# Performance work log

Hardware: AMD Instinct MI355X
Metric: run time of the kernel (lower is better)

## Reference

```python
import jax, jax.numpy as jnp
import numpy as np

N = 8192          # num nodes
F_IN = 512        # num_features
H = 256           # hidden_dim
D = 64            # embedding_dim
E = 262144        # num edges (avg degree 32)


def setup_inputs() -> dict:
    key = jax.random.key(0)
    ks = jax.random.split(key, 6)
    x = jax.random.normal(ks[0], (N, F_IN), dtype=jnp.float32)
    adj_rows = jax.random.randint(ks[1], (E,), 0, N)
    adj_cols = jax.random.randint(ks[2], (E,), 0, N)
    adj_vals = jax.random.uniform(ks[3], (E,), dtype=jnp.float32)
    W1 = jax.random.normal(ks[4], (F_IN, H), dtype=jnp.float32) / np.sqrt(F_IN)
    b1 = jnp.zeros((H,), dtype=jnp.float32)
    W2 = jax.random.normal(ks[5], (H, D), dtype=jnp.float32) / np.sqrt(H)
    b2 = jnp.zeros((D,), dtype=jnp.float32)
    return {"x": x, "adj_rows": adj_rows, "adj_cols": adj_cols,
            "adj_vals": adj_vals, "W1": W1, "b1": b1, "W2": W2, "b2": b2}


def _spmm(rows, cols, vals, dense):
    # sparse [N,N] @ dense [N,F] via gather + segment-sum (COO spmm)
    gathered = vals[:, None] * dense[cols]           # [E, F]
    return jax.ops.segment_sum(gathered, rows, num_segments=N)


def reference(x, adj_rows, adj_cols, adj_vals, W1, b1, W2, b2):
    # GCN layer 1: linear -> spmm -> relu (dropout is identity in eval mode)
    h = _spmm(adj_rows, adj_cols, adj_vals, x @ W1 + b1)   # [N, H]
    h = jax.nn.relu(h)
    # GCN layer 2: linear -> spmm
    z = _spmm(adj_rows, adj_cols, adj_vals, h @ W2 + b2)   # [N, D]
    # decode: sigmoid(z z^T)
    adj_rec = jax.nn.sigmoid(z @ z.T)                       # [N, N]
    return (z, adj_rec)
```

## Files before the change

kernel.cpp:

```cpp
#include <hip/hip_runtime.h>
#include <hip/hip_bf16.h>

#define NN 8192
#define FIN 512
#define HD 256
#define DD 64
#define NE 262144
#define BCAP 128

typedef __bf16 bf16_t;
typedef __bf16 bf16x8 __attribute__((ext_vector_type(8)));
typedef __bf16 bf16x4 __attribute__((ext_vector_type(4)));
typedef float f32x4 __attribute__((ext_vector_type(4)));

__global__ __launch_bounds__(256) void prep_kernel(const float* __restrict__ x, bf16_t* __restrict__ x_b,
                                                   const float* __restrict__ W1, bf16_t* __restrict__ w1t,
                                                   const float* __restrict__ W2, bf16_t* __restrict__ w2t,
                                                   int* __restrict__ deg) {
    int b = blockIdx.x;
    if (b < 4096) {
        int i = (b * 256 + threadIdx.x) * 4;
        float4 v = *reinterpret_cast<const float4*>(x + i);
        x_b[i + 0] = (bf16_t)v.x;
        x_b[i + 1] = (bf16_t)v.y;
        x_b[i + 2] = (bf16_t)v.z;
        x_b[i + 3] = (bf16_t)v.w;
    } else if (b < 4096 + 512) {
        int o = (b - 4096) * 256 + threadIdx.x;
        int r = o & 511;
        int c = o >> 9;
        w1t[o] = (bf16_t)W1[r * HD + c];
    } else if (b < 4096 + 512 + 64) {
        int o = (b - 4096 - 512) * 256 + threadIdx.x;
        int r = o & 255;
        int c = o >> 8;
        w2t[o] = (bf16_t)W2[r * DD + c];
    } else {
        int o = (b - 4096 - 512 - 64) * 256 + threadIdx.x;
        deg[o] = 0;
    }
}


__global__ void scatter_edges(const int* __restrict__ rows, const int* __restrict__ cols,
                              const float* __restrict__ vals,
                              int* __restrict__ deg, int2* __restrict__ sedge) {
    int e = blockIdx.x * blockDim.x + threadIdx.x;
    if (e < NE) {
        int r = rows[e];
        int p = atomicAdd(&deg[r], 1);
        int2 pk;
        pk.x = cols[e];
        pk.y = __float_as_int(vals[e]);
        sedge[r * BCAP + p] = pk;
    }
}


__global__ __launch_bounds__(256) void spmm_h_kernel(const int* __restrict__ deg,
                                                     const int2* __restrict__ sedge,
                                                     const bf16_t* __restrict__ h0,
                                                     bf16_t* __restrict__ h) {
    int wv = threadIdx.x >> 6;
    int lane = threadIdx.x & 63;
    int r = blockIdx.x * 4 + wv;
    int nd = deg[r];
    int base = r * BCAP;
    __shared__ int2 ecS[4][64];
    float a0 = 0.f, a1 = 0.f, a2 = 0.f, a3 = 0.f;
    for (int e0 = 0; e0 < nd; e0 += 64) {
        int rem = nd - e0;
        if (rem > 64) rem = 64;
        if (lane < rem) ecS[wv][lane] = sedge[base + e0 + lane];
#pragma unroll 4
        for (int e = 0; e < rem; e++) {
            int c = ecS[wv][e].x;
            float v = __int_as_float(ecS[wv][e].y);
            bf16x4 hv = *reinterpret_cast<const bf16x4*>(h0 + (size_t)c * HD + lane * 4);
            a0 += v * (float)hv[0];
            a1 += v * (float)hv[1];
            a2 += v * (float)hv[2];
            a3 += v * (float)hv[3];
        }
    }
    bf16x4 o;
    o[0] = (bf16_t)fmaxf(a0, 0.f);
    o[1] = (bf16_t)fmaxf(a1, 0.f);
    o[2] = (bf16_t)fmaxf(a2, 0.f);
    o[3] = (bf16_t)fmaxf(a3, 0.f);
    *reinterpret_cast<bf16x4*>(h + (size_t)r * HD + lane * 4) = o;
}

__global__ __launch_bounds__(256) void spmm_z_kernel(const int* __restrict__ deg,
                                                     const int2* __restrict__ sedge,
                                                     const bf16_t* __restrict__ z0,
                                                     float* __restrict__ z_out,
                                                     bf16_t* __restrict__ z_b) {
    int wv = threadIdx.x >> 6;
    int lane = threadIdx.x & 63;
    int r = blockIdx.x * 4 + wv;
    int sub = lane >> 4;
    int fl = lane & 15;
    int nd = deg[r];
    int base = r * BCAP;
    __shared__ int2 ecS[4][64];
    float a0 = 0.f, a1 = 0.f, a2 = 0.f, a3 = 0.f;
    for (int e0 = 0; e0 < nd; e0 += 64) {
        int rem = nd - e0;
        if (rem > 64) rem = 64;
        if (lane < rem) ecS[wv][lane] = sedge[base + e0 + lane];
#pragma unroll 4
        for (int e = sub; e < rem; e += 4) {
            int c = ecS[wv][e].x;
            float v = __int_as_float(ecS[wv][e].y);
            bf16x4 zv = *reinterpret_cast<const bf16x4*>(z0 + (size_t)c * DD + fl * 4);
            a0 += v * (float)zv[0];
            a1 += v * (float)zv[1];
            a2 += v * (float)zv[2];
            a3 += v * (float)zv[3];
        }
    }
    a0 += __shfl_xor(a0, 16); a0 += __shfl_xor(a0, 32);
    a1 += __shfl_xor(a1, 16); a1 += __shfl_xor(a1, 32);
    a2 += __shfl_xor(a2, 16); a2 += __shfl_xor(a2, 32);
    a3 += __shfl_xor(a3, 16); a3 += __shfl_xor(a3, 32);
    if (sub == 0) {
        f32x4 o = {a0, a1, a2, a3};
        *reinterpret_cast<f32x4*>(z_out + (size_t)r * DD + fl * 4) = o;
        bf16x4 ob;
        ob[0] = (bf16_t)a0; ob[1] = (bf16_t)a1; ob[2] = (bf16_t)a2; ob[3] = (bf16_t)a3;
        *reinterpret_cast<bf16x4*>(z_b + (size_t)r * DD + fl * 4) = ob;
    }
}

template <int ACT, typename OutT, int MW, int NT>
__global__ __launch_bounds__(256) void gemm_bt(const bf16_t* __restrict__ A,
                                               const bf16_t* __restrict__ Bt,
                                               const float* __restrict__ bias,
                                               OutT* __restrict__ C,
                                               int M, int N, int K) {
    int wave = threadIdx.x >> 6;
    int lane = threadIdx.x & 63;
    int lr = lane & 15;
    int lq = lane >> 4;
    int bm = (ACT == 2) ? blockIdx.y : blockIdx.x;
    int bn = (ACT == 2) ? blockIdx.x : blockIdx.y;
    int mblk = bm * (64 * MW);
    int m0 = mblk + wave * (16 * MW);
    int n0 = bn * (16 * NT);

    f32x4 acc[MW][NT];
#pragma unroll
    for (int i = 0; i < MW; i++)
#pragma unroll
        for (int t = 0; t < NT; t++) acc[i][t] = {0.f, 0.f, 0.f, 0.f};

    const bf16_t* Abase = A + (size_t)(m0 + lr) * K + lq * 8;
    const bf16_t* Bbase = Bt + (size_t)(n0 + lr) * K + lq * 8;

    for (int k0 = 0; k0 < K; k0 += 32) {
        bf16x8 a[MW];
#pragma unroll
        for (int i = 0; i < MW; i++)
            a[i] = *reinterpret_cast<const bf16x8*>(Abase + (size_t)i * 16 * K + k0);
#pragma unroll
        for (int t = 0; t < NT; t++) {
            bf16x8 b = *reinterpret_cast<const bf16x8*>(Bbase + (size_t)t * 16 * K + k0);
#pragma unroll
            for (int i = 0; i < MW; i++)
                acc[i][t] = __builtin_amdgcn_mfma_f32_16x16x32_bf16(a[i], b, acc[i][t], 0, 0, 0);
        }
    }

    if (ACT == 2) {
        __shared__ float ldsT[4][16][65];
        int c4 = (lane & 15) * 4;
        int rr = lane >> 4;
#pragma unroll
        for (int i = 0; i < MW; i++) {
#pragma unroll
            for (int t = 0; t < 4; t++)
#pragma unroll
                for (int r = 0; r < 4; r++) {
                    float v = acc[i][t][r];
                    v = 1.f / (1.f + __expf(-v));
                    ldsT[wave][lq * 4 + r][t * 16 + lr] = v;
                }
#pragma unroll
            for (int j = 0; j < 4; j++) {
                int row_l = j * 4 + rr;
                f32x4 v = *reinterpret_cast<const f32x4*>(&ldsT[wave][row_l][c4]);
                size_t grow = (size_t)(m0 + i * 16 + row_l);
                *reinterpret_cast<f32x4*>(&C[grow * N + n0 + c4]) = v;
            }
        }
    } else {
#pragma unroll
        for (int i = 0; i < MW; i++) {
#pragma unroll
            for (int t = 0; t < NT; t++) {
                int col = n0 + t * 16 + lr;
                float bv = bias ? bias[col] : 0.f;
#pragma unroll
                for (int r = 0; r < 4; r++) {
                    int row = m0 + i * 16 + lq * 4 + r;
                    C[(size_t)row * N + col] = (OutT)(acc[i][t][r] + bv);
                }
            }
        }
    }
}


extern "C" void kernel_launch(void* const* d_in, const int* in_sizes, int n_in,
                              void* d_out, int out_size, void* d_ws, size_t ws_size,
                              hipStream_t stream) {
    const float* x   = (const float*)d_in[0];
    const int* rows  = (const int*)d_in[1];
    const int* cols  = (const int*)d_in[2];
    const float* vals = (const float*)d_in[3];
    const float* W1  = (const float*)d_in[4];
    const float* b1  = (const float*)d_in[5];
    const float* W2  = (const float*)d_in[6];
    const float* b2  = (const float*)d_in[7];

    float* out_z   = (float*)d_out;
    float* out_adj = out_z + (size_t)NN * DD;

    char* ws = (char*)d_ws;
    size_t off = 0;
    auto alloc = [&](size_t bytes) { void* p = ws + off; off += (bytes + 255) & ~(size_t)255; return p; };
    bf16_t* x_b   = (bf16_t*)alloc((size_t)NN * FIN * 2);
    bf16_t* w1t   = (bf16_t*)alloc((size_t)HD * FIN * 2);
    bf16_t* w2t   = (bf16_t*)alloc((size_t)DD * HD * 2);
    bf16_t* h0    = (bf16_t*)alloc((size_t)NN * HD * 2);
    bf16_t* h_b   = (bf16_t*)alloc((size_t)NN * HD * 2);
    bf16_t* z0    = (bf16_t*)alloc((size_t)NN * DD * 2);
    bf16_t* z_b   = (bf16_t*)alloc((size_t)NN * DD * 2);
    int* deg      = (int*)alloc((size_t)NN * 4);
    int2* sedge   = (int2*)alloc((size_t)NN * BCAP * 8);

    prep_kernel<<<4096 + 512 + 64 + 32, 256, 0, stream>>>(x, x_b, W1, w1t, W2, w2t, deg);

    scatter_edges<<<NE / 256, 256, 0, stream>>>(rows, cols, vals, deg, sedge);

    gemm_bt<0, bf16_t, 1, 4><<<dim3(NN / 64, HD / 64), 256, 0, stream>>>(x_b, w1t, b1, h0, NN, HD, FIN);

    spmm_h_kernel<<<NN / 4, 256, 0, stream>>>(deg, sedge, h0, h_b);

    gemm_bt<0, bf16_t, 1, 4><<<dim3(NN / 64, DD / 64), 256, 0, stream>>>(h_b, w2t, b2, z0, NN, DD, HD);

    spmm_z_kernel<<<NN / 4, 256, 0, stream>>>(deg, sedge, z0, out_z, z_b);

    gemm_bt<2, float, 2, 4><<<dim3(NN / 64, NN / 128), 256, 0, stream>>>(z_b, z_b, nullptr, out_adj, NN, NN, DD);
}
```

Baseline: 368.3 us.

## Fuse first-layer SpMM with second-layer GEMM via shared-memory tile and MFMA

Merges the layer-1 SpMM+ReLU kernel with the h@W2+b2 GEMM. Each block now aggregates 16 rows into shared memory and multiplies them by W2 with bf16 MFMA instructions. This removes the h intermediate's write and read through global memory and one kernel launch. In exchange there are 4x fewer blocks, each wave processes 4 rows serially, and a block barrier sits before the GEMM, which could reduce latency hiding in the gather.

Result: no change. 369.8 us (+0.4%).

```diff
diff --git a/kernel.cpp b/kernel.cpp
--- a/kernel.cpp
+++ b/kernel.cpp
@@ -56,39 +56,65 @@
     }
 }
 
-
-__global__ __launch_bounds__(256) void spmm_h_kernel(const int* __restrict__ deg,
-                                                     const int2* __restrict__ sedge,
-                                                     const bf16_t* __restrict__ h0,
-                                                     bf16_t* __restrict__ h) {
+__global__ __launch_bounds__(256) void spmm_h_gemm2_kernel(const int* __restrict__ deg,
+                                                           const int2* __restrict__ sedge,
+                                                           const bf16_t* __restrict__ h0,
+                                                           const bf16_t* __restrict__ w2t,
+                                                           const float* __restrict__ b2,
+                                                           bf16_t* __restrict__ z0) {
     int wv = threadIdx.x >> 6;
     int lane = threadIdx.x & 63;
-    int r = blockIdx.x * 4 + wv;
-    int nd = deg[r];
-    int base = r * BCAP;
+    int r0 = blockIdx.x * 16;
     __shared__ int2 ecS[4][64];
-    float a0 = 0.f, a1 = 0.f, a2 = 0.f, a3 = 0.f;
-    for (int e0 = 0; e0 < nd; e0 += 64) {
-        int rem = nd - e0;
-        if (rem > 64) rem = 64;
-        if (lane < rem) ecS[wv][lane] = sedge[base + e0 + lane];
+    __shared__ bf16_t hS[16][264];
+
+#pragma unroll
+    for (int i = 0; i < 4; i++) {
+        int r = r0 + wv * 4 + i;
+        int nd = deg[r];
+        int base = r * BCAP;
+        float a0 = 0.f, a1 = 0.f, a2 = 0.f, a3 = 0.f;
+        for (int e0 = 0; e0 < nd; e0 += 64) {
+            int rem = nd - e0;
+            if (rem > 64) rem = 64;
+            if (lane < rem) ecS[wv][lane] = sedge[base + e0 + lane];
 #pragma unroll 4
-        for (int e = 0; e < rem; e++) {
-            int c = ecS[wv][e].x;
-            float v = __int_as_float(ecS[wv][e].y);
-            bf16x4 hv = *reinterpret_cast<const bf16x4*>(h0 + (size_t)c * HD + lane * 4);
-            a0 += v * (float)hv[0];
-            a1 += v * (float)hv[1];
-            a2 += v * (float)hv[2];
-            a3 += v * (float)hv[3];
-        }
-    }
-    bf16x4 o;
-    o[0] = (bf16_t)fmaxf(a0, 0.f);
-    o[1] = (bf16_t)fmaxf(a1, 0.f);
-    o[2] = (bf16_t)fmaxf(a2, 0.f);
-    o[3] = (bf16_t)fmaxf(a3, 0.f);
-    *reinterpret_cast<bf16x4*>(h + (size_t)r * HD + lane * 4) = o;
+            for (int e = 0; e < rem; e++) {
+                int c = ecS[wv][e].x;
+                float v = __int_as_float(ecS[wv][e].y);
+                bf16x4 hv = *reinterpret_cast<const bf16x4*>(h0 + (size_t)c * HD + lane * 4);
+                a0 += v * (float)hv[0];
+                a1 += v * (float)hv[1];
+                a2 += v * (float)hv[2];
+                a3 += v * (float)hv[3];
+            }
+        }
+        bf16x4 o;
+        o[0] = (bf16_t)fmaxf(a0, 0.f);
+        o[1] = (bf16_t)fmaxf(a1, 0.f);
+        o[2] = (bf16_t)fmaxf(a2, 0.f);
+        o[3] = (bf16_t)fmaxf(a3, 0.f);
+        *reinterpret_cast<bf16x4*>(&hS[wv * 4 + i][lane * 4]) = o;
+    }
+    __syncthreads();
+
+    int lr = lane & 15;
+    int lq = lane >> 4;
+    f32x4 zacc = {0.f, 0.f, 0.f, 0.f};
+    const bf16_t* brow = w2t + (size_t)(wv * 16 + lr) * HD + lq * 8;
+#pragma unroll
+    for (int k0 = 0; k0 < HD; k0 += 32) {
+        bf16x8 a = *reinterpret_cast<const bf16x8*>(&hS[lr][k0 + lq * 8]);
+        bf16x8 b = *reinterpret_cast<const bf16x8*>(brow + k0);
+        zacc = __builtin_amdgcn_mfma_f32_16x16x32_bf16(a, b, zacc, 0, 0, 0);
+    }
+    int c = wv * 16 + lr;
+    float bv = b2[c];
+#pragma unroll
+    for (int r = 0; r < 4; r++) {
+        int row = lq * 4 + r;
+        z0[(size_t)(r0 + row) * DD + c] = (bf16_t)(zacc[r] + bv);
+    }
 }
 
 __global__ __launch_bounds__(256) void spmm_z_kernel(const int* __restrict__ deg,
@@ -234,7 +260,6 @@
     bf16_t* w1t   = (bf16_t*)alloc((size_t)HD * FIN * 2);
     bf16_t* w2t   = (bf16_t*)alloc((size_t)DD * HD * 2);
     bf16_t* h0    = (bf16_t*)alloc((size_t)NN * HD * 2);
-    bf16_t* h_b   = (bf16_t*)alloc((size_t)NN * HD * 2);
     bf16_t* z0    = (bf16_t*)alloc((size_t)NN * DD * 2);
     bf16_t* z_b   = (bf16_t*)alloc((size_t)NN * DD * 2);
     int* deg      = (int*)alloc((size_t)NN * 4);
@@ -246,9 +271,7 @@
 
     gemm_bt<0, bf16_t, 1, 4><<<dim3(NN / 64, HD / 64), 256, 0, stream>>>(x_b, w1t, b1, h0, NN, HD, FIN);
 
-    spmm_h_kernel<<<NN / 4, 256, 0, stream>>>(deg, sedge, h0, h_b);
-
-    gemm_bt<0, bf16_t, 1, 4><<<dim3(NN / 64, DD / 64), 256, 0, stream>>>(h_b, w2t, b2, z0, NN, DD, HD);
+    spmm_h_gemm2_kernel<<<NN / 16, 256, 0, stream>>>(deg, sedge, h0, w2t, b2, z0);
 
     spmm_z_kernel<<<NN / 4, 256, 0, stream>>>(deg, sedge, z0, out_z, z_b);
 
```
